# Kernel tuning notes

Hardware: AMD Instinct MI355X
Metric: run time of the kernel (lower is better)

## Reference

```python
import jax, jax.numpy as jnp
import numpy as np

NEG_SLOPE = 0.2


def setup_inputs() -> dict:
    key = jax.random.key(0)
    ks = jax.random.split(key, 6)
    N, E, IN, OUT = 100000, 1600000, 128, 64
    x = jax.random.normal(ks[0], (N, IN), dtype=jnp.float32)
    edge_index = jax.random.randint(ks[1], (2, E), 0, N, dtype=jnp.int64)
    W = jax.random.normal(ks[2], (IN, OUT), dtype=jnp.float32) * (1.0 / np.sqrt(IN))
    att_src = jax.random.normal(ks[3], (OUT,), dtype=jnp.float32) * (1.0 / np.sqrt(OUT))
    att_dst = jax.random.normal(ks[4], (OUT,), dtype=jnp.float32) * (1.0 / np.sqrt(OUT))
    bias = jnp.zeros((OUT,), dtype=jnp.float32)
    return {"x": x, "edge_index": edge_index, "W": W,
            "att_src": att_src, "att_dst": att_dst, "bias": bias}


def reference(x, edge_index, W, att_src, att_dst, bias):
    N = x.shape[0]
    # PyG GATConv default: add self loops
    loop = jnp.arange(N, dtype=edge_index.dtype)
    src = jnp.concatenate([edge_index[0], loop])  # message sources j
    dst = jnp.concatenate([edge_index[1], loop])  # message targets i

    h = x @ W                                      # [N, out]
    a_s = h @ att_src                              # [N]
    a_d = h @ att_dst                              # [N]

    # per-edge unnormalized attention logits (leaky relu, slope 0.2)
    e = jax.nn.leaky_relu(a_s[src] + a_d[dst], negative_slope=NEG_SLOPE)  # [E+N]

    # segment softmax over edges grouped by destination node
    seg_max = jax.ops.segment_max(e, dst, num_segments=N)  # [N]
    e_exp = jnp.exp(e - seg_max[dst])
    seg_sum = jax.ops.segment_sum(e_exp, dst, num_segments=N)  # [N], >0 via self loops
    alpha = e_exp / seg_sum[dst]                                # [E+N]

    # weighted scatter-add aggregation
    out = jax.ops.segment_sum(alpha[:, None] * h[src], dst, num_segments=N)  # [N, out]
    return out + bias
```

## Files before the change

### kernel.cpp

```cpp
#include <hip/hip_runtime.h>
#include <hip/hip_bf16.h>
#include <math.h>

#define NEG_SLOPE 0.2f
#define BSH    7
#define BNODES 128
#define CAP    4096
#define MAXB   1024
#define NCHUNK 512
#define CEMAX  3200

typedef __attribute__((ext_vector_type(8))) short bf16x8;
typedef __attribute__((ext_vector_type(4))) float f32x4;

__device__ __forceinline__ float leaky(float v) { return v >= 0.0f ? v : NEG_SLOPE * v; }
__device__ __forceinline__ int clampi(int v, int lo, int hi) {
    return v < lo ? lo : (v > hi ? hi : v);
}
__device__ __forceinline__ float bflo(unsigned u) { return __uint_as_float(u << 16); }
__device__ __forceinline__ float bfhi(unsigned u) { return __uint_as_float(u & 0xFFFF0000u); }
__device__ __forceinline__ unsigned short f2bf(float f) {
    unsigned u = __float_as_uint(f);
    return (unsigned short)((u + 0x7FFFu + ((u >> 16) & 1u)) >> 16);
}
__device__ __forceinline__ bf16x8 pack8(float4 a, float4 b) {
    bf16x8 r;
    r[0] = (short)f2bf(a.x); r[1] = (short)f2bf(a.y);
    r[2] = (short)f2bf(a.z); r[3] = (short)f2bf(a.w);
    r[4] = (short)f2bf(b.x); r[5] = (short)f2bf(b.y);
    r[6] = (short)f2bf(b.z); r[7] = (short)f2bf(b.w);
    return r;
}

__global__ __launch_bounds__(512) void k_linear(
    const float* __restrict__ x, const float* __restrict__ W,
    const float* __restrict__ att_src, const float* __restrict__ att_dst,
    __hip_bfloat16* __restrict__ h, float* __restrict__ a_s,
    float* __restrict__ a_d, int N)
{
    __shared__ short wlds[16 * 64 * 8];

    const int tid = threadIdx.x;
    for (int idx = tid; idx < 1024; idx += 512) {
        int f = idx >> 6, L = idx & 63;
        int t = f >> 2, k0i = f & 3;
        int kbase = k0i * 32 + (L >> 4) * 8;
        int c = t * 16 + (L & 15);
        unsigned short v[8];
#pragma unroll
        for (int j = 0; j < 8; ++j) v[j] = f2bf(W[(kbase + j) * 64 + c]);
        uint4 p;
        p.x = (unsigned)v[0] | ((unsigned)v[1] << 16);
        p.y = (unsigned)v[2] | ((unsigned)v[3] << 16);
        p.z = (unsigned)v[4] | ((unsigned)v[5] << 16);
        p.w = (unsigned)v[6] | ((unsigned)v[7] << 16);
        ((uint4*)wlds)[idx] = p;
    }
    __syncthreads();

    const int lane = tid & 63;
    const int w    = tid >> 6;
    const int base = blockIdx.x * 128 + w * 16;
    const int m    = lane & 15;
    const int quad = lane >> 4;

    int rowc = min(base + m, N - 1);
    const float4* xr = (const float4*)x + (size_t)rowc * 32;

    bf16x8 afrag[4];
#pragma unroll
    for (int k0i = 0; k0i < 4; ++k0i) {
        float4 f0 = xr[k0i * 8 + quad * 2 + 0];
        float4 f1 = xr[k0i * 8 + quad * 2 + 1];
        afrag[k0i] = pack8(f0, f1);
    }

    f32x4 acc[4];
#pragma unroll
    for (int t = 0; t < 4; ++t) acc[t] = (f32x4){0.f, 0.f, 0.f, 0.f};

    const bf16x8* wf = (const bf16x8*)wlds;
#pragma unroll
    for (int t = 0; t < 4; ++t) {
#pragma unroll
        for (int k0i = 0; k0i < 4; ++k0i) {
            bf16x8 b = wf[(t * 4 + k0i) * 64 + lane];
            acc[t] = __builtin_amdgcn_mfma_f32_16x16x32_bf16(afrag[k0i], b, acc[t], 0, 0, 0);
        }
    }

    float ps[4] = {0.f, 0.f, 0.f, 0.f};
    float pd[4] = {0.f, 0.f, 0.f, 0.f};
#pragma unroll
    for (int t = 0; t < 4; ++t) {
        float as_c = att_src[t * 16 + m];
        float ad_c = att_dst[t * 16 + m];
#pragma unroll
        for (int q = 0; q < 4; ++q) {
            ps[q] = fmaf(acc[t][q], as_c, ps[q]);
            pd[q] = fmaf(acc[t][q], ad_c, pd[q]);
        }
    }
#pragma unroll
    for (int t = 0; t < 4; ++t) {
#pragma unroll
        for (int q = 0; q < 4; ++q) {
            int n = base + quad * 4 + q;
            if (n < N) h[(size_t)n * 64 + t * 16 + m] = __float2bfloat16(acc[t][q]);
        }
    }
#pragma unroll
    for (int q = 0; q < 4; ++q) {
        ps[q] += __shfl_xor(ps[q], 1, 64);
        ps[q] += __shfl_xor(ps[q], 2, 64);
        ps[q] += __shfl_xor(ps[q], 4, 64);
        ps[q] += __shfl_xor(ps[q], 8, 64);
        pd[q] += __shfl_xor(pd[q], 1, 64);
        pd[q] += __shfl_xor(pd[q], 2, 64);
        pd[q] += __shfl_xor(pd[q], 4, 64);
        pd[q] += __shfl_xor(pd[q], 8, 64);
    }
    if (m == 0) {
#pragma unroll
        for (int q = 0; q < 4; ++q) {
            int n = base + quad * 4 + q;
            if (n < N) { a_s[n] = ps[q]; a_d[n] = pd[q]; }
        }
    }
}

__global__ __launch_bounds__(512) void k_part2(
    const int* __restrict__ ei, unsigned* __restrict__ binned,
    int* __restrict__ offc, int E, int N, int CE)
{
    __shared__ int hist[MAXB];
    __shared__ int off[MAXB];
    __shared__ int cur[MAXB];
    __shared__ int s[512];
    __shared__ unsigned stage[CEMAX];

    const int c   = blockIdx.x;
    const int tid = threadIdx.x;
    const int e0  = c * CE;
    const int e1  = min(E, e0 + CE);
    const int ne  = e1 - e0;

    for (int i = tid; i < MAXB; i += 512) hist[i] = 0;
    __syncthreads();
    for (int e = e0 + tid; e < e1; e += 512) {
        int dst = clampi(ei[E + e], 0, N - 1);
        atomicAdd(&hist[dst >> BSH], 1);
    }
    __syncthreads();
    int a0 = hist[2 * tid], a1 = hist[2 * tid + 1];
    int psum = a0 + a1;
    s[tid] = psum;
    __syncthreads();
    for (int d = 1; d < 512; d <<= 1) {
        int v = (tid >= d) ? s[tid - d] : 0;
        __syncthreads();
        s[tid] += v;
        __syncthreads();
    }
    int excl = s[tid] - psum;
    off[2 * tid]     = excl;
    off[2 * tid + 1] = excl + a0;
    cur[2 * tid]     = excl;
    cur[2 * tid + 1] = excl + a0;
    __syncthreads();
    for (int e = e0 + tid; e < e1; e += 512) {
        int src = clampi(ei[e],     0, N - 1);
        int dst = clampi(ei[E + e], 0, N - 1);
        int pos = atomicAdd(&cur[dst >> BSH], 1);
        stage[clampi(pos, 0, CEMAX - 1)] =
            ((unsigned)(dst & (BNODES - 1)) << 17) | (unsigned)src;
    }
    __syncthreads();
    for (int i = tid; i < ne; i += 512) binned[e0 + i] = stage[i];
    int* oc = offc + (size_t)c * (MAXB + 1);
    for (int i = tid; i < MAXB; i += 512) oc[i] = off[i];
    if (tid == 0) oc[MAXB] = ne;
}

__global__ __launch_bounds__(512) void k_agg(
    const unsigned* __restrict__ binned, const int* __restrict__ offc,
    const float* __restrict__ a_s, const float* __restrict__ a_d,
    const __hip_bfloat16* __restrict__ hm, const float* __restrict__ bias,
    float* __restrict__ out, int N, int CE)
{
    __shared__ int   cnt[BNODES];
    __shared__ int   st[BNODES];
    __shared__ int   cur[BNODES];
    __shared__ float lsum[BNODES];
    __shared__ float wsl[BNODES];
    __shared__ float adl[BNODES];
    __shared__ uint2 ew[CAP];

    const int tid   = threadIdx.x;
    const int b     = blockIdx.x;
    const int nbase = b << BSH;

    if (tid < BNODES) {
        cnt[tid] = 0;
        int n = nbase + tid;
        float as = 0.f, ad = 0.f;
        if (n < N) { as = a_s[n]; ad = a_d[n]; }
        adl[tid] = ad;
        float v = (n < N) ? __expf(leaky(as + ad)) : 0.f;
        wsl[tid]  = v;
        lsum[tid] = v;
    }
    int rbase = 0, rcnt = 0;
    if (tid < NCHUNK) {
        const int* oc = offc + (size_t)tid * (MAXB + 1);
        int o0 = clampi(oc[b],     0, CE);
        int o1 = clampi(oc[b + 1], o0, CE);
        rbase = tid * CE + o0;
        rcnt  = o1 - o0;
    }
    __syncthreads();
    for (int i = 0; i < rcnt; ++i) {
        unsigned pk = binned[rbase + i];
        atomicAdd(&cnt[(pk >> 17) & (BNODES - 1)], 1);
    }
    __syncthreads();
    if (tid < BNODES) st[tid] = cnt[tid];
    __syncthreads();
    for (int d = 1; d < BNODES; d <<= 1) {
        int v = (tid < BNODES && tid >= d) ? st[tid - d] : 0;
        __syncthreads();
        if (tid < BNODES) st[tid] += v;
        __syncthreads();
    }
    if (tid < BNODES) { st[tid] -= cnt[tid]; cur[tid] = st[tid]; }
    __syncthreads();
    for (int i = 0; i < rcnt; ++i) {
        unsigned pk = binned[rbase + i];
        int ld  = (int)(pk >> 17) & (BNODES - 1);
        int src = (int)(pk & 0x1FFFFu);
        float wv = __expf(leaky(a_s[src] + adl[ld]));
        int pos = atomicAdd(&cur[ld], 1);
        if (pos < CAP) ew[pos] = make_uint2((unsigned)src, __float_as_uint(wv));
        atomicAdd(&lsum[ld], wv);
    }
    __syncthreads();

    const int lane = tid & 63;
    const int w    = tid >> 6;
    const int q    = lane & 7;
    const int p    = lane >> 3;
    const uint4*  h4 = (const uint4*)hm;
    const float4* b4 = (const float4*)bias;
    const float4 bb0 = b4[2 * q];
    const float4 bb1 = b4[2 * q + 1];

#pragma unroll 1
    for (int t = 0; t < 2; ++t) {
        int ln = t * 64 + w * 8 + p;
        int n  = nbase + ln;
        if (n >= N) continue;
        int deg = cnt[ln];
        int s0  = st[ln];
        if (s0 > CAP) s0 = CAP;
        if (deg > CAP - s0) deg = CAP - s0;

        float wself = wsl[ln];
        uint4 U = h4[(size_t)n * 8 + q];
        float acc0 = wself * bflo(U.x), acc1 = wself * bfhi(U.x);
        float acc2 = wself * bflo(U.y), acc3 = wself * bfhi(U.y);
        float acc4 = wself * bflo(U.z), acc5 = wself * bfhi(U.z);
        float acc6 = wself * bflo(U.w), acc7 = wself * bfhi(U.w);

        float wc = 0.f;
        if (deg > 0) {
            uint2 e0 = ew[s0];
            wc = __uint_as_float(e0.y);
            U  = h4[(size_t)e0.x * 8 + q];
        }
        for (int j = 0; j < deg; ++j) {
            uint4 U2 = make_uint4(0u, 0u, 0u, 0u);
            float w2 = 0.f;
            if (j + 1 < deg) {
                uint2 e1 = ew[s0 + j + 1];
                w2 = __uint_as_float(e1.y);
                U2 = h4[(size_t)e1.x * 8 + q];
            }
            acc0 = fmaf(wc, bflo(U.x), acc0);
            acc1 = fmaf(wc, bfhi(U.x), acc1);
            acc2 = fmaf(wc, bflo(U.y), acc2);
            acc3 = fmaf(wc, bfhi(U.y), acc3);
            acc4 = fmaf(wc, bflo(U.z), acc4);
            acc5 = fmaf(wc, bfhi(U.z), acc5);
            acc6 = fmaf(wc, bflo(U.w), acc6);
            acc7 = fmaf(wc, bfhi(U.w), acc7);
            U = U2; wc = w2;
        }

        float inv = 1.0f / lsum[ln];
        float4 o0, o1;
        o0.x = bb0.x + acc0 * inv;
        o0.y = bb0.y + acc1 * inv;
        o0.z = bb0.z + acc2 * inv;
        o0.w = bb0.w + acc3 * inv;
        o1.x = bb1.x + acc4 * inv;
        o1.y = bb1.y + acc5 * inv;
        o1.z = bb1.z + acc6 * inv;
        o1.w = bb1.w + acc7 * inv;
        float4* o4 = (float4*)out;
        o4[(size_t)n * 16 + 2 * q + 0] = o0;
        o4[(size_t)n * 16 + 2 * q + 1] = o1;
    }
}

extern "C" void kernel_launch(void* const* d_in, const int* in_sizes, int n_in,
                              void* d_out, int out_size, void* d_ws, size_t ws_size,
                              hipStream_t stream)
{
    const float* x       = (const float*)d_in[0];
    const int*   ei      = (const int*)d_in[1];
    const float* W       = (const float*)d_in[2];
    const float* att_src = (const float*)d_in[3];
    const float* att_dst = (const float*)d_in[4];
    const float* bias    = (const float*)d_in[5];
    float*       out     = (float*)d_out;

    const int N = in_sizes[0] / 128;
    const int E = in_sizes[1] / 2;

    __hip_bfloat16* h      = (__hip_bfloat16*)d_ws;
    float*          a_s    = (float*)(h + (size_t)N * 64);
    float*          a_d    = a_s + N;
    int*            offc   = (int*)(a_d + N);
    unsigned*       binned = (unsigned*)(offc + NCHUNK * (MAXB + 1));

    const int CE = (E + NCHUNK - 1) / NCHUNK;
    const int NB = (N + BNODES - 1) >> BSH;

    int nb_lin = (N + 127) / 128;

    k_linear<<<nb_lin, 512, 0, stream>>>(x, W, att_src, att_dst, h, a_s, a_d, N);
    k_part2 <<<NCHUNK, 512, 0, stream>>>(ei, binned, offc, E, N, CE);
    k_agg   <<<NB,     512, 0, stream>>>(binned, offc, a_s, a_d, h, bias, out, N, CE);
}
```

Baseline: 187.5 us.

## Fuse linear and partition kernels; gather binned edges cooperatively in aggregation

Merges the linear projection and edge partitioning into one launch, using a block-index split so both run concurrently and one launch is saved. Halves the number of partition chunks, which doubles the edges per chunk and grows the staging buffer. In the aggregation kernel, the serial per-thread walk over each chunk's run is replaced by a prefix scan over run lengths, a binary search, and a block-wide coalesced gather into LDS, which spreads the loads evenly across threads. Risks include higher LDS use lowering occupancy, and the smaller CAP of 2560 may truncate edges for heavily loaded node bins.

```diff
diff --git a/kernel.cpp b/kernel.cpp
--- a/kernel.cpp
+++ b/kernel.cpp
@@ -5,10 +5,11 @@
 #define NEG_SLOPE 0.2f
 #define BSH    7
 #define BNODES 128
-#define CAP    4096
+#define CAP    2560
 #define MAXB   1024
-#define NCHUNK 512
-#define CEMAX  3200
+#define NCHUNK 256
+#define CEMAX  6272
+#define SMEMB  39424
 
 typedef __attribute__((ext_vector_type(8))) short bf16x8;
 typedef __attribute__((ext_vector_type(4))) float f32x4;
@@ -32,154 +33,154 @@
     return r;
 }
 
-__global__ __launch_bounds__(512) void k_linear(
+__global__ __launch_bounds__(512) void k_fused(
     const float* __restrict__ x, const float* __restrict__ W,
     const float* __restrict__ att_src, const float* __restrict__ att_dst,
     __hip_bfloat16* __restrict__ h, float* __restrict__ a_s,
-    float* __restrict__ a_d, int N)
+    float* __restrict__ a_d, const int* __restrict__ ei,
+    unsigned* __restrict__ binned, int* __restrict__ offc,
+    int N, int E, int CE, int nb_lin)
 {
-    __shared__ short wlds[16 * 64 * 8];
-
+    __shared__ int4 smem4[SMEMB / 16];
     const int tid = threadIdx.x;
-    for (int idx = tid; idx < 1024; idx += 512) {
-        int f = idx >> 6, L = idx & 63;
-        int t = f >> 2, k0i = f & 3;
-        int kbase = k0i * 32 + (L >> 4) * 8;
-        int c = t * 16 + (L & 15);
-        unsigned short v[8];
-#pragma unroll
-        for (int j = 0; j < 8; ++j) v[j] = f2bf(W[(kbase + j) * 64 + c]);
-        uint4 p;
-        p.x = (unsigned)v[0] | ((unsigned)v[1] << 16);
-        p.y = (unsigned)v[2] | ((unsigned)v[3] << 16);
-        p.z = (unsigned)v[4] | ((unsigned)v[5] << 16);
-        p.w = (unsigned)v[6] | ((unsigned)v[7] << 16);
-        ((uint4*)wlds)[idx] = p;
-    }
-    __syncthreads();
-
-    const int lane = tid & 63;
-    const int w    = tid >> 6;
-    const int base = blockIdx.x * 128 + w * 16;
-    const int m    = lane & 15;
-    const int quad = lane >> 4;
-
-    int rowc = min(base + m, N - 1);
-    const float4* xr = (const float4*)x + (size_t)rowc * 32;
-
-    bf16x8 afrag[4];
-#pragma unroll
-    for (int k0i = 0; k0i < 4; ++k0i) {
-        float4 f0 = xr[k0i * 8 + quad * 2 + 0];
-        float4 f1 = xr[k0i * 8 + quad * 2 + 1];
-        afrag[k0i] = pack8(f0, f1);
-    }
-
-    f32x4 acc[4];
-#pragma unroll
-    for (int t = 0; t < 4; ++t) acc[t] = (f32x4){0.f, 0.f, 0.f, 0.f};
-
-    const bf16x8* wf = (const bf16x8*)wlds;
-#pragma unroll
-    for (int t = 0; t < 4; ++t) {
+
+    if ((int)blockIdx.x < nb_lin) {
+        short* wlds = (short*)smem4;
+
+        for (int idx = tid; idx < 1024; idx += 512) {
+            int f = idx >> 6, L = idx & 63;
+            int t = f >> 2, k0i = f & 3;
+            int kbase = k0i * 32 + (L >> 4) * 8;
+            int c = t * 16 + (L & 15);
+            unsigned short v[8];
+#pragma unroll
+            for (int j = 0; j < 8; ++j) v[j] = f2bf(W[(kbase + j) * 64 + c]);
+            uint4 p;
+            p.x = (unsigned)v[0] | ((unsigned)v[1] << 16);
+            p.y = (unsigned)v[2] | ((unsigned)v[3] << 16);
+            p.z = (unsigned)v[4] | ((unsigned)v[5] << 16);
+            p.w = (unsigned)v[6] | ((unsigned)v[7] << 16);
+            ((uint4*)wlds)[idx] = p;
+        }
+        __syncthreads();
+
+        const int lane = tid & 63;
+        const int w    = tid >> 6;
+        const int base = blockIdx.x * 128 + w * 16;
+        const int m    = lane & 15;
+        const int quad = lane >> 4;
+
+        int rowc = min(base + m, N - 1);
+        const float4* xr = (const float4*)x + (size_t)rowc * 32;
+
+        bf16x8 afrag[4];
 #pragma unroll
         for (int k0i = 0; k0i < 4; ++k0i) {
-            bf16x8 b = wf[(t * 4 + k0i) * 64 + lane];
-            acc[t] = __builtin_amdgcn_mfma_f32_16x16x32_bf16(afrag[k0i], b, acc[t], 0, 0, 0);
-        }
-    }
-
-    float ps[4] = {0.f, 0.f, 0.f, 0.f};
-    float pd[4] = {0.f, 0.f, 0.f, 0.f};
-#pragma unroll
-    for (int t = 0; t < 4; ++t) {
-        float as_c = att_src[t * 16 + m];
-        float ad_c = att_dst[t * 16 + m];
+            float4 f0 = xr[k0i * 8 + quad * 2 + 0];
+            float4 f1 = xr[k0i * 8 + quad * 2 + 1];
+            afrag[k0i] = pack8(f0, f1);
+        }
+
+        f32x4 acc[4];
+#pragma unroll
+        for (int t = 0; t < 4; ++t) acc[t] = (f32x4){0.f, 0.f, 0.f, 0.f};
+
+        const bf16x8* wf = (const bf16x8*)wlds;
+#pragma unroll
+        for (int t = 0; t < 4; ++t) {
+#pragma unroll
+            for (int k0i = 0; k0i < 4; ++k0i) {
+                bf16x8 bfr = wf[(t * 4 + k0i) * 64 + lane];
+                acc[t] = __builtin_amdgcn_mfma_f32_16x16x32_bf16(afrag[k0i], bfr, acc[t], 0, 0, 0);
+            }
+        }
+
+        float ps[4] = {0.f, 0.f, 0.f, 0.f};
+        float pd[4] = {0.f, 0.f, 0.f, 0.f};
+#pragma unroll
+        for (int t = 0; t < 4; ++t) {
+            float as_c = att_src[t * 16 + m];
+            float ad_c = att_dst[t * 16 + m];
+#pragma unroll
+            for (int q = 0; q < 4; ++q) {
+                ps[q] = fmaf(acc[t][q], as_c, ps[q]);
+                pd[q] = fmaf(acc[t][q], ad_c, pd[q]);
+            }
+        }
+#pragma unroll
+        for (int t = 0; t < 4; ++t) {
+#pragma unroll
+            for (int q = 0; q < 4; ++q) {
+                int n = base + quad * 4 + q;
+                if (n < N) h[(size_t)n * 64 + t * 16 + m] = __float2bfloat16(acc[t][q]);
+            }
+        }
 #pragma unroll
         for (int q = 0; q < 4; ++q) {
-            ps[q] = fmaf(acc[t][q], as_c, ps[q]);
-            pd[q] = fmaf(acc[t][q], ad_c, pd[q]);
-        }
-    }
-#pragma unroll
-    for (int t = 0; t < 4; ++t) {
-#pragma unroll
-        for (int q = 0; q < 4; ++q) {
-            int n = base + quad * 4 + q;
-            if (n < N) h[(size_t)n * 64 + t * 16 + m] = __float2bfloat16(acc[t][q]);
-        }
-    }
-#pragma unroll
-    for (int q = 0; q < 4; ++q) {
-        ps[q] += __shfl_xor(ps[q], 1, 64);
-        ps[q] += __shfl_xor(ps[q], 2, 64);
-        ps[q] += __shfl_xor(ps[q], 4, 64);
-        ps[q] += __shfl_xor(ps[q], 8, 64);
-        pd[q] += __shfl_xor(pd[q], 1, 64);
-        pd[q] += __shfl_xor(pd[q], 2, 64);
-        pd[q] += __shfl_xor(pd[q], 4, 64);
-        pd[q] += __shfl_xor(pd[q], 8, 64);
-    }
-    if (m == 0) {
-#pragma unroll
-        for (int q = 0; q < 4; ++q) {
-            int n = base + quad * 4 + q;
-            if (n < N) { a_s[n] = ps[q]; a_d[n] = pd[q]; }
-        }
-    }
-}
-
-__global__ __launch_bounds__(512) void k_part2(
-    const int* __restrict__ ei, unsigned* __restrict__ binned,
-    int* __restrict__ offc, int E, int N, int CE)
-{
-    __shared__ int hist[MAXB];
-    __shared__ int off[MAXB];
-    __shared__ int cur[MAXB];
-    __shared__ int s[512];
-    __shared__ unsigned stage[CEMAX];
-
-    const int c   = blockIdx.x;
-    const int tid = threadIdx.x;
-    const int e0  = c * CE;
-    const int e1  = min(E, e0 + CE);
-    const int ne  = e1 - e0;
-
-    for (int i = tid; i < MAXB; i += 512) hist[i] = 0;
-    __syncthreads();
-    for (int e = e0 + tid; e < e1; e += 512) {
-        int dst = clampi(ei[E + e], 0, N - 1);
-        atomicAdd(&hist[dst >> BSH], 1);
-    }
-    __syncthreads();
-    int a0 = hist[2 * tid], a1 = hist[2 * tid + 1];
-    int psum = a0 + a1;
-    s[tid] = psum;
-    __syncthreads();
-    for (int d = 1; d < 512; d <<= 1) {
-        int v = (tid >= d) ? s[tid - d] : 0;
-        __syncthreads();
-        s[tid] += v;
-        __syncthreads();
-    }
-    int excl = s[tid] - psum;
-    off[2 * tid]     = excl;
-    off[2 * tid + 1] = excl + a0;
-    cur[2 * tid]     = excl;
-    cur[2 * tid + 1] = excl + a0;
-    __syncthreads();
-    for (int e = e0 + tid; e < e1; e += 512) {
-        int src = clampi(ei[e],     0, N - 1);
-        int dst = clampi(ei[E + e], 0, N - 1);
-        int pos = atomicAdd(&cur[dst >> BSH], 1);
-        stage[clampi(pos, 0, CEMAX - 1)] =
-            ((unsigned)(dst & (BNODES - 1)) << 17) | (unsigned)src;
-    }
-    __syncthreads();
-    for (int i = tid; i < ne; i += 512) binned[e0 + i] = stage[i];
-    int* oc = offc + (size_t)c * (MAXB + 1);
-    for (int i = tid; i < MAXB; i += 512) oc[i] = off[i];
-    if (tid == 0) oc[MAXB] = ne;
+            ps[q] += __shfl_xor(ps[q], 1, 64);
+            ps[q] += __shfl_xor(ps[q], 2, 64);
+            ps[q] += __shfl_xor(ps[q], 4, 64);
+            ps[q] += __shfl_xor(ps[q], 8, 64);
+            pd[q] += __shfl_xor(pd[q], 1, 64);
+            pd[q] += __shfl_xor(pd[q], 2, 64);
+            pd[q] += __shfl_xor(pd[q], 4, 64);
+            pd[q] += __shfl_xor(pd[q], 8, 64);
+        }
+        if (m == 0) {
+#pragma unroll
+            for (int q = 0; q < 4; ++q) {
+                int n = base + quad * 4 + q;
+                if (n < N) { a_s[n] = ps[q]; a_d[n] = pd[q]; }
+            }
+        }
+    } else {
+        int* hist = (int*)smem4;
+        int* off  = hist + MAXB;
+        int* cur  = off + MAXB;
+        int* s    = cur + MAXB;
+        unsigned* stage = (unsigned*)(s + 512);
+
+        const int c  = (int)blockIdx.x - nb_lin;
+        const int e0 = c * CE;
+        const int e1 = min(E, e0 + CE);
+        const int ne = e1 - e0;
+
+        for (int i = tid; i < MAXB; i += 512) hist[i] = 0;
+        __syncthreads();
+        for (int e = e0 + tid; e < e1; e += 512) {
+            int dst = clampi(ei[E + e], 0, N - 1);
+            atomicAdd(&hist[dst >> BSH], 1);
+        }
+        __syncthreads();
+        int a0 = hist[2 * tid], a1 = hist[2 * tid + 1];
+        int psum = a0 + a1;
+        s[tid] = psum;
+        __syncthreads();
+        for (int d = 1; d < 512; d <<= 1) {
+            int v = (tid >= d) ? s[tid - d] : 0;
+            __syncthreads();
+            s[tid] += v;
+            __syncthreads();
+        }
+        int excl = s[tid] - psum;
+        off[2 * tid]     = excl;
+        off[2 * tid + 1] = excl + a0;
+        cur[2 * tid]     = excl;
+        cur[2 * tid + 1] = excl + a0;
+        __syncthreads();
+        for (int e = e0 + tid; e < e1; e += 512) {
+            int src = clampi(ei[e],     0, N - 1);
+            int dst = clampi(ei[E + e], 0, N - 1);
+            int pos = atomicAdd(&cur[dst >> BSH], 1);
+            stage[clampi(pos, 0, CEMAX - 1)] =
+                ((unsigned)(dst & (BNODES - 1)) << 17) | (unsigned)src;
+        }
+        __syncthreads();
+        for (int i = tid; i < ne; i += 512) binned[e0 + i] = stage[i];
+        int* oc = offc + (size_t)c * (MAXB + 1);
+        for (int i = tid; i < MAXB; i += 512) oc[i] = off[i];
+        if (tid == 0) oc[MAXB] = ne;
+    }
 }
 
 __global__ __launch_bounds__(512) void k_agg(
@@ -194,6 +195,10 @@
     __shared__ float lsum[BNODES];
     __shared__ float wsl[BNODES];
     __shared__ float adl[BNODES];
+    __shared__ int   runScan[NCHUNK + 1];
+    __shared__ int   gbase[NCHUNK];
+    __shared__ int   sc[NCHUNK];
+    __shared__ unsigned eraw[CAP];
     __shared__ uint2 ew[CAP];
 
     const int tid   = threadIdx.x;
@@ -210,19 +215,38 @@
         wsl[tid]  = v;
         lsum[tid] = v;
     }
-    int rbase = 0, rcnt = 0;
+    int rc = 0;
     if (tid < NCHUNK) {
         const int* oc = offc + (size_t)tid * (MAXB + 1);
         int o0 = clampi(oc[b],     0, CE);
         int o1 = clampi(oc[b + 1], o0, CE);
-        rbase = tid * CE + o0;
-        rcnt  = o1 - o0;
-    }
-    __syncthreads();
-    for (int i = 0; i < rcnt; ++i) {
-        unsigned pk = binned[rbase + i];
-        atomicAdd(&cnt[(pk >> 17) & (BNODES - 1)], 1);
-    }
+        rc = o1 - o0;
+        gbase[tid] = tid * CE + o0;
+        sc[tid] = rc;
+    }
+    __syncthreads();
+    for (int d = 1; d < NCHUNK; d <<= 1) {
+        int v = (tid < NCHUNK && tid >= d) ? sc[tid - d] : 0;
+        __syncthreads();
+        if (tid < NCHUNK) sc[tid] += v;
+        __syncthreads();
+    }
+    if (tid < NCHUNK) runScan[tid] = sc[tid] - rc;
+    if (tid == NCHUNK - 1) runScan[NCHUNK] = sc[NCHUNK - 1];
+    __syncthreads();
+    int n_e = runScan[NCHUNK];
+    if (n_e > CAP) n_e = CAP;
+
+    for (int i = tid; i < n_e; i += 512) {
+        int c = 0;
+#pragma unroll
+        for (int stp = NCHUNK >> 1; stp >= 1; stp >>= 1)
+            if (runScan[c + stp] <= i) c += stp;
+        eraw[i] = binned[(size_t)gbase[c] + (i - runScan[c])];
+    }
+    __syncthreads();
+    for (int i = tid; i < n_e; i += 512)
+        atomicAdd(&cnt[(eraw[i] >> 17) & (BNODES - 1)], 1);
     __syncthreads();
     if (tid < BNODES) st[tid] = cnt[tid];
     __syncthreads();
@@ -234,8 +258,8 @@
     }
     if (tid < BNODES) { st[tid] -= cnt[tid]; cur[tid] = st[tid]; }
     __syncthreads();
-    for (int i = 0; i < rcnt; ++i) {
-        unsigned pk = binned[rbase + i];
+    for (int i = tid; i < n_e; i += 512) {
+        unsigned pk = eraw[i];
         int ld  = (int)(pk >> 17) & (BNODES - 1);
         int src = (int)(pk & 0x1FFFFu);
         float wv = __expf(leaky(a_s[src] + adl[ld]));
@@ -335,10 +359,11 @@
 
     const int CE = (E + NCHUNK - 1) / NCHUNK;
     const int NB = (N + BNODES - 1) >> BSH;
-
-    int nb_lin = (N + 127) / 128;
-
-    k_linear<<<nb_lin, 512, 0, stream>>>(x, W, att_src, att_dst, h, a_s, a_d, N);
-    k_part2 <<<NCHUNK, 512, 0, stream>>>(ei, binned, offc, E, N, CE);
-    k_agg   <<<NB,     512, 0, stream>>>(binned, offc, a_s, a_d, h, bias, out, N, CE);
-}
+    const int nb_lin = (N + 127) / 128;
+
+    k_fused<<<nb_lin + NCHUNK, 512, 0, stream>>>(x, W, att_src, att_dst,
+                                                 h, a_s, a_d, ei, binned, offc,
+                                                 N, E, CE, nb_lin);
+    k_agg  <<<NB,              512, 0, stream>>>(binned, offc, a_s, a_d, h,
+                                                 bias, out, N, CE);
+}
```

New measurement: 168.8 us. -10.0%, faster.
